# Optimization experiments

Hardware: AMD Instinct MI355X
Metric: run time of the kernel (lower is better)

The kernel has to match this reference:

```python
import jax, jax.numpy as jnp
import numpy as np

D_IN = 1024
D_OUT = 1024
NUM_HEADS = 16
HEAD_DIM = D_OUT // NUM_HEADS


def setup_inputs() -> dict:
    key = jax.random.key(0)
    ks = jax.random.split(key, 6)
    s = 0.02
    return {
        "x": jax.random.normal(ks[0], (4, 2048, D_IN), dtype=jnp.float32),
        "Wq": jax.random.normal(ks[1], (D_IN, D_OUT), dtype=jnp.float32) * s,
        "Wk": jax.random.normal(ks[2], (D_IN, D_OUT), dtype=jnp.float32) * s,
        "Wv": jax.random.normal(ks[3], (D_IN, D_OUT), dtype=jnp.float32) * s,
        "Wo": jax.random.normal(ks[4], (D_OUT, D_OUT), dtype=jnp.float32) * s,
        "bo": jax.random.normal(ks[5], (D_OUT,), dtype=jnp.float32) * s,
    }


def reference(x, Wq, Wk, Wv, Wo, bo):
    B, T, _ = x.shape
    H, Dh = NUM_HEADS, HEAD_DIM
    # projections -> [B, H, T, Dh]
    q = (x @ Wq).reshape(B, T, H, Dh).transpose(0, 2, 1, 3)
    k = (x @ Wk).reshape(B, T, H, Dh).transpose(0, 2, 1, 3)
    v = (x @ Wv).reshape(B, T, H, Dh).transpose(0, 2, 1, 3)
    # scores [B, H, T, T]
    scores = jnp.einsum('bhqd,bhkd->bhqk', q, k)
    causal = jnp.triu(jnp.ones((T, T), dtype=bool), k=1)
    scores = jnp.where(causal, -jnp.inf, scores)
    attn = jax.nn.softmax(scores / jnp.sqrt(jnp.float32(Dh)), axis=-1)
    # dropout=0.0 -> identity
    ctx = jnp.einsum('bhqk,bhkd->bhqd', attn, v)
    ctx = ctx.transpose(0, 2, 1, 3).reshape(B, T, H * Dh)
    return ctx @ Wo + bo
```

## Files before the change

### kernel.cpp

```cpp
#include <hip/hip_runtime.h>
#include <hip/hip_bf16.h>
#include <stdint.h>

#define TSEQ 2048
#define DMODEL 1024

typedef __attribute__((ext_vector_type(8))) short bf16x8;
typedef __attribute__((ext_vector_type(4))) float f32x4;
typedef __attribute__((ext_vector_type(16))) float f32x16;

union Frag { bf16x8 v; uint4 q; };

__device__ __forceinline__ uint16_t f2bfu(float f) {
  uint32_t u = __builtin_bit_cast(uint32_t, f);
  u += 0x7fffu + ((u >> 16) & 1u);
  return (uint16_t)(u >> 16);
}

__device__ __forceinline__ uint32_t pk2bf(float a, float b) {
  return ((uint32_t)f2bfu(b) << 16) | f2bfu(a);
}

__device__ __forceinline__ float fexp2(float x) {
#if __has_builtin(__builtin_amdgcn_exp2f)
  return __builtin_amdgcn_exp2f(x);
#else
  return exp2f(x);
#endif
}

__device__ __forceinline__ void gload_lds16(const void* g, void* l) {
  __builtin_amdgcn_global_load_lds(
      (const __attribute__((address_space(1))) void*)g,
      (__attribute__((address_space(3))) void*)l, 16, 0, 0);
}


__global__ __launch_bounds__(256) void cvt_x_kernel(const float* __restrict__ x,
                                                    uint16_t* __restrict__ xb, int n4) {
  int i = blockIdx.x * 256 + threadIdx.x;
  if (i >= n4) return;
  float4 v = ((const float4*)x)[i];
  ushort4 o;
  o.x = f2bfu(v.x); o.y = f2bfu(v.y); o.z = f2bfu(v.z); o.w = f2bfu(v.w);
  ((ushort4*)xb)[i] = o;
}

__global__ __launch_bounds__(256) void cvt_w_kernel(const float* __restrict__ Wq,
    const float* __restrict__ Wk, const float* __restrict__ Wv, const float* __restrict__ Wo,
    uint16_t* __restrict__ Wqkvt, uint16_t* __restrict__ Wot) {
  const float* src = (blockIdx.z == 0) ? Wq : (blockIdx.z == 1) ? Wk
                   : (blockIdx.z == 2) ? Wv : Wo;
  uint16_t* dst = (blockIdx.z < 3) ? (Wqkvt + (size_t)blockIdx.z * DMODEL * DMODEL) : Wot;
  const float wscale = (blockIdx.z == 0) ? 0.125f * 1.4426950408889634f : 1.0f;
  __shared__ float tile[32][33];
  const int x0 = blockIdx.x * 32, y0 = blockIdx.y * 32;
  for (int ii = 0; ii < 4; ii++) {
    int i = threadIdx.y + ii * 8;
    tile[i][threadIdx.x] = src[(size_t)(y0 + i) * DMODEL + x0 + threadIdx.x];
  }
  __syncthreads();
  for (int ii = 0; ii < 4; ii++) {
    int i = threadIdx.y + ii * 8;
    dst[(size_t)(x0 + i) * DMODEL + y0 + threadIdx.x] = f2bfu(tile[threadIdx.x][i] * wscale);
  }
}


__device__ __forceinline__ void g8_stage_p1(const char* Ab, int kb, char* ldsA, int tid) {
#pragma unroll
  for (int r = 0; r < 3; ++r) {
    const int u = tid + r * 512;
    const int row = u >> 3;
    const int sc = ((u & 7) * 16) ^ ((row & 7) << 4);
    gload_lds16(Ab + (size_t)row * 2048 + kb + sc, ldsA + u * 16);
  }
}

__device__ __forceinline__ void g8_stage_p2(const char* Ab, const char* Bb, int kb,
                                            char* ldsA, char* ldsB, int tid) {
  {
    const int u = tid + 3 * 512;
    const int row = u >> 3;
    const int sc = ((u & 7) * 16) ^ ((row & 7) << 4);
    gload_lds16(Ab + (size_t)row * 2048 + kb + sc, ldsA + u * 16);
  }
#pragma unroll
  for (int r = 0; r < 2; ++r) {
    const int u = tid + r * 512;
    const int row = u >> 3;
    const int sc = ((u & 7) * 16) ^ ((row & 7) << 4);
    gload_lds16(Bb + (size_t)row * 2048 + kb + sc, ldsB + u * 16);
  }
}

__device__ __forceinline__ void gemm256x128_core(const char* Ab, const char* Bb,
                                                 char* lds,
                                                 f32x4 (&acc)[4][4]) {
  const int tid = threadIdx.x;
  const int lane = tid & 63;
  const int w = tid >> 6;
  const int lr = lane & 15, lg = lane >> 4;
  const int wmb = (w >> 1) * 64;
  const int wnb = (w & 1) * 64;
  char* const A0 = lds;
  char* const A1 = lds + 32768;
  char* const B0 = lds + 65536;
  char* const B1 = lds + 81920;

#pragma unroll
  for (int i = 0; i < 4; i++)
#pragma unroll
    for (int j = 0; j < 4; j++) acc[i][j] = (f32x4){0.f, 0.f, 0.f, 0.f};

  g8_stage_p1(Ab, 0, A0, tid);
  g8_stage_p2(Ab, Bb, 0, A0, B0, tid);
  for (int t = 0; t < 16; ++t) {
    const char* At = (t & 1) ? A1 : A0;
    const char* Bt = (t & 1) ? B1 : B0;
    char* nA = (t & 1) ? A0 : A1;
    char* nB = (t & 1) ? B0 : B1;
    if (t + 1 < 16) {
      g8_stage_p1(Ab, (t + 1) * 128, nA, tid);
      asm volatile("s_waitcnt vmcnt(3)" ::: "memory");
    } else {
      asm volatile("s_waitcnt vmcnt(0)" ::: "memory");
    }
    __builtin_amdgcn_s_barrier();
    __builtin_amdgcn_sched_barrier(0);

    Frag bf0[4], bf1[4];
#pragma unroll
    for (int ni = 0; ni < 4; ni++) {
      const int row = wnb + ni * 16 + lr;
      const int swz = (row & 7) << 4;
      bf0[ni].q = *(const uint4*)(Bt + row * 128 + ((lg * 16) ^ swz));
      bf1[ni].q = *(const uint4*)(Bt + row * 128 + ((64 + lg * 16) ^ swz));
    }
    Frag pa0[2], pa1[2];
#pragma unroll
    for (int mi = 0; mi < 2; mi++) {
      const int row = wmb + mi * 16 + lr;
      const int swz = (row & 7) << 4;
      pa0[mi].q = *(const uint4*)(At + row * 128 + ((lg * 16) ^ swz));
      pa1[mi].q = *(const uint4*)(At + row * 128 + ((64 + lg * 16) ^ swz));
    }
    __builtin_amdgcn_s_setprio(1);
#pragma unroll
    for (int mi = 0; mi < 2; mi++)
#pragma unroll
      for (int ni = 0; ni < 4; ni++) {
        acc[mi][ni] = __builtin_amdgcn_mfma_f32_16x16x32_bf16(pa0[mi].v, bf0[ni].v,
                                                              acc[mi][ni], 0, 0, 0);
        acc[mi][ni] = __builtin_amdgcn_mfma_f32_16x16x32_bf16(pa1[mi].v, bf1[ni].v,
                                                              acc[mi][ni], 0, 0, 0);
      }
    __builtin_amdgcn_s_setprio(0);

    if (t + 1 < 16) g8_stage_p2(Ab, Bb, (t + 1) * 128, nA, nB, tid);
#pragma unroll
    for (int mi = 2; mi < 4; mi++) {
      const int row = wmb + mi * 16 + lr;
      const int swz = (row & 7) << 4;
      Frag qa0, qa1;
      qa0.q = *(const uint4*)(At + row * 128 + ((lg * 16) ^ swz));
      qa1.q = *(const uint4*)(At + row * 128 + ((64 + lg * 16) ^ swz));
      __builtin_amdgcn_s_setprio(1);
#pragma unroll
      for (int ni = 0; ni < 4; ni++) {
        acc[mi][ni] = __builtin_amdgcn_mfma_f32_16x16x32_bf16(qa0.v, bf0[ni].v,
                                                              acc[mi][ni], 0, 0, 0);
        acc[mi][ni] = __builtin_amdgcn_mfma_f32_16x16x32_bf16(qa1.v, bf1[ni].v,
                                                              acc[mi][ni], 0, 0, 0);
      }
      __builtin_amdgcn_s_setprio(0);
    }
    __builtin_amdgcn_s_barrier();
  }
}


__global__ __launch_bounds__(512, 2) void gemm_qkv_kernel(const uint16_t* __restrict__ Xb,
    const uint16_t* __restrict__ Wt, uint16_t* __restrict__ Qo,
    uint16_t* __restrict__ Ko, uint16_t* __restrict__ Vt) {
  __shared__ __align__(16) char lds[98304];
  const int m0 = (blockIdx.x & 31) * 256;
  const int n0 = (blockIdx.x >> 5) * 128;
  f32x4 acc[4][4];
  gemm256x128_core((const char*)Xb + (size_t)m0 * 2048, (const char*)Wt + (size_t)n0 * 2048,
                   lds, acc);

  const int tid = threadIdx.x, w = tid >> 6, lane = tid & 63;
  const int lr = lane & 15, lg = lane >> 4;
  const int wmb = (w >> 1) * 64, wnb = (w & 1) * 64;

  if (n0 >= 2048) {
    char* vr = lds + (w & 1) * 33792;
#pragma unroll
    for (int mi = 0; mi < 4; mi++)
#pragma unroll
      for (int ni = 0; ni < 4; ni++) {
        const int d = ni * 16 + lr;
        const int tl = wmb + mi * 16 + 4 * lg;
        uint2 pr;
        pr.x = pk2bf(acc[mi][ni][0], acc[mi][ni][1]);
        pr.y = pk2bf(acc[mi][ni][2], acc[mi][ni][3]);
        *(uint2*)(vr + d * 528 + tl * 2) = pr;
      }
    __syncthreads();
    const int bb = m0 >> 11, t0 = m0 & 2047;
    const int h0 = (n0 - 2048) >> 6;
#pragma unroll
    for (int j = 0; j < 8; j++) {
      const int linear = (tid + j * 512) * 16;
      const int rg = linear >> 15;
      const int rem = linear & 32767;
      const int d = rem >> 9;
      const int toff = rem & 511;
      const uint4 val = *(const uint4*)(lds + rg * 33792 + d * 528 + toff);
      const int bh = bb * 16 + h0 + rg;
      *(uint4*)((char*)Vt + ((size_t)(bh * 64 + d) * TSEQ + t0) * 2 + toff) = val;
    }
  } else {
#pragma unroll
    for (int mi = 0; mi < 4; mi++)
#pragma unroll
      for (int ni = 0; ni < 4; ni++) {
        const int col = n0 + wnb + ni * 16 + lr;
        const int p = col >> 10, c = col & 1023, h = c >> 6, d = c & 63;
#pragma unroll
        for (int r = 0; r < 4; r++) {
          const int row = m0 + wmb + mi * 16 + 4 * lg + r;
          const int bb = row >> 11, t = row & 2047;
          const int bh = bb * 16 + h;
          const uint16_t val = f2bfu(acc[mi][ni][r]);
          if (p == 0) Qo[((size_t)bh * TSEQ + t) * 64 + d] = val;
          else        Ko[((size_t)bh * TSEQ + t) * 64 + d] = val;
        }
      }
  }
}


__device__ __forceinline__ void stage_kv(const char* Kb, const char* Vb, int kv0,
                                         char* kdst, char* vdst, int tid) {
  const int w1024 = (tid >> 6) * 1024;
#pragma unroll
  for (int i = 0; i < 2; i++) {
    const int o = i * 4096 + tid * 16;
    const int row = o >> 7;
    const int scol = (o & 127) ^ ((row & 7) << 4);
    gload_lds16(Kb + (size_t)(kv0 + row) * 128 + scol, kdst + i * 4096 + w1024);
    gload_lds16(Vb + (size_t)row * 4096 + kv0 * 2 + scol, vdst + i * 4096 + w1024);
  }
}

__global__ __launch_bounds__(256, 3) void attn_kernel(const uint16_t* __restrict__ Qw,
    const uint16_t* __restrict__ Kw, const uint16_t* __restrict__ Vtw,
    uint16_t* __restrict__ Ctx) {
  const int bid = blockIdx.x;
  const int qt = 15 - (bid >> 6);
  const int bh = bid & 63;
  const int tid = threadIdx.x;
  const int w = tid >> 6, lane = tid & 63;
  const int lq = lane & 31;
  const int hi = lane >> 5;
  const int wq0 = qt * 128 + w * 32;

  const char* Qb = (const char*)Qw + (size_t)bh * TSEQ * 128;
  const char* Kb = (const char*)Kw + (size_t)bh * TSEQ * 128;
  const char* Vb = (const char*)Vtw + (size_t)bh * 64 * 4096;

  __shared__ __align__(16) char kbuf[2][8192];
  __shared__ __align__(16) char vbuf[2][8192];

  Frag qa[4];
#pragma unroll
  for (int kc = 0; kc < 4; kc++)
    qa[kc].q = *(const uint4*)(Qb + (size_t)(wq0 + lq) * 128 + kc * 32 + hi * 16);

  f32x16 o0 = 0.f, o1 = 0.f;
  float mrun = -1e30f, lrun = 0.f;

  const int nt = 2 * qt + 2;
  stage_kv(Kb, Vb, 0, kbuf[0], vbuf[0], tid);
  int cur = 0;
  for (int t = 0; t < nt; ++t) {
    const int kv0 = t * 64;
    if (t + 1 < nt) {
      stage_kv(Kb, Vb, kv0 + 64, kbuf[cur ^ 1], vbuf[cur ^ 1], tid);
      asm volatile("s_waitcnt vmcnt(4)" ::: "memory");
    } else {
      asm volatile("s_waitcnt vmcnt(0)" ::: "memory");
    }
    __builtin_amdgcn_s_barrier();
    __builtin_amdgcn_sched_barrier(0);

    if (kv0 <= wq0 + 31) {
      const char* Kt = kbuf[cur];
      const char* Vt = vbuf[cur];
      f32x16 s[2];
#pragma unroll
      for (int kvh = 0; kvh < 2; kvh++) {
        f32x16 acc = 0.f;
#pragma unroll
        for (int kc = 0; kc < 4; kc++) {
          const int row = kvh * 32 + lq;
          Frag kf;
          kf.q = *(const uint4*)(Kt + row * 128 + ((kc * 32 + hi * 16) ^ ((row & 7) << 4)));
          acc = __builtin_amdgcn_mfma_f32_32x32x16_bf16(kf.v, qa[kc].v, acc, 0, 0, 0);
        }
        s[kvh] = acc;
      }
      if (kv0 + 63 > wq0) {
        const int q_abs = wq0 + lq;
#pragma unroll
        for (int kvh = 0; kvh < 2; kvh++)
#pragma unroll
          for (int r = 0; r < 16; r++) {
            const int kv_abs = kv0 + kvh * 32 + (r & 3) + 8 * (r >> 2) + 4 * hi;
            if (kv_abs > q_abs) s[kvh][r] = -1e30f;
          }
      }
      float mt = s[0][0];
#pragma unroll
      for (int r = 1; r < 16; r++) mt = fmaxf(mt, s[0][r]);
#pragma unroll
      for (int r = 0; r < 16; r++) mt = fmaxf(mt, s[1][r]);
      mt = fmaxf(mt, __shfl_xor(mt, 32));
      const float mnew = fmaxf(mrun, mt);
      const float corr = fexp2(mrun - mnew);
      mrun = mnew;
#pragma unroll
      for (int kvh = 0; kvh < 2; kvh++)
#pragma unroll
        for (int r = 0; r < 16; r++) s[kvh][r] = fexp2(s[kvh][r] - mnew);
      float ps = 0.f;
#pragma unroll
      for (int kvh = 0; kvh < 2; kvh++)
#pragma unroll
        for (int r = 0; r < 16; r++) ps += s[kvh][r];
      ps += __shfl_xor(ps, 32);
      lrun = lrun * corr + ps;
      o0 *= corr;
      o1 *= corr;
      uint32_t pk[2][8];
#pragma unroll
      for (int kvh = 0; kvh < 2; kvh++)
#pragma unroll
        for (int j = 0; j < 8; j++)
          pk[kvh][j] = pk2bf(s[kvh][2 * j], s[kvh][2 * j + 1]);
#pragma unroll
      for (int c16 = 0; c16 < 4; c16++) {
        const int kvh = c16 >> 1, cl = c16 & 1;
        const uint32_t s0 = (uint32_t)__shfl_xor((int)pk[kvh][4 * cl + 0], 32);
        const uint32_t s1 = (uint32_t)__shfl_xor((int)pk[kvh][4 * cl + 1], 32);
        const uint32_t s2 = (uint32_t)__shfl_xor((int)pk[kvh][4 * cl + 2], 32);
        const uint32_t s3 = (uint32_t)__shfl_xor((int)pk[kvh][4 * cl + 3], 32);
        Frag pb;
        pb.q.x = hi ? s2 : pk[kvh][4 * cl + 0];
        pb.q.y = hi ? s3 : pk[kvh][4 * cl + 1];
        pb.q.z = hi ? pk[kvh][4 * cl + 2] : s0;
        pb.q.w = hi ? pk[kvh][4 * cl + 3] : s1;
#pragma unroll
        for (int dblk = 0; dblk < 2; dblk++) {
          const int row = dblk * 32 + lq;
          Frag vf;
          vf.q = *(const uint4*)(Vt + row * 128 + ((c16 * 32 + hi * 16) ^ ((row & 7) << 4)));
          if (dblk == 0)
            o0 = __builtin_amdgcn_mfma_f32_32x32x16_bf16(vf.v, pb.v, o0, 0, 0, 0);
          else
            o1 = __builtin_amdgcn_mfma_f32_32x32x16_bf16(vf.v, pb.v, o1, 0, 0, 0);
        }
      }
    }
    __builtin_amdgcn_s_barrier();
    cur ^= 1;
  }

  const int bb = bh >> 4, hh = bh & 15;
  const float inv = 1.0f / lrun;
  const int q_abs = wq0 + lq;
  uint16_t* crow = Ctx + ((size_t)bb * TSEQ + q_abs) * DMODEL + hh * 64;
#pragma unroll
  for (int dblk = 0; dblk < 2; dblk++)
#pragma unroll
    for (int g = 0; g < 4; g++) {
      const float a0 = (dblk ? o1[4 * g + 0] : o0[4 * g + 0]) * inv;
      const float a1 = (dblk ? o1[4 * g + 1] : o0[4 * g + 1]) * inv;
      const float a2 = (dblk ? o1[4 * g + 2] : o0[4 * g + 2]) * inv;
      const float a3 = (dblk ? o1[4 * g + 3] : o0[4 * g + 3]) * inv;
      uint2 st;
      st.x = pk2bf(a0, a1);
      st.y = pk2bf(a2, a3);
      *(uint2*)(crow + dblk * 32 + 8 * g + 4 * hi) = st;
    }
}


__global__ __launch_bounds__(512, 2) void gemm_out_kernel(const uint16_t* __restrict__ Cb,
    const uint16_t* __restrict__ Wot, const float* __restrict__ bo,
    float* __restrict__ out) {
  __shared__ __align__(16) char lds[98304];
  const int m0 = (blockIdx.x & 31) * 256;
  const int n0 = (blockIdx.x >> 5) * 128;
  f32x4 acc[4][4];
  gemm256x128_core((const char*)Cb + (size_t)m0 * 2048, (const char*)Wot + (size_t)n0 * 2048,
                   lds, acc);

  const int tid = threadIdx.x, w = tid >> 6, lane = tid & 63;
  const int lr = lane & 15, lg = lane >> 4;
  const int wmb = (w >> 1) * 64, wnb = (w & 1) * 64;
#pragma unroll
  for (int mi = 0; mi < 4; mi++)
#pragma unroll
    for (int ni = 0; ni < 4; ni++) {
      const int col = n0 + wnb + ni * 16 + lr;
      const float bias = bo[col];
#pragma unroll
      for (int r = 0; r < 4; r++) {
        const int row = m0 + wmb + mi * 16 + 4 * lg + r;
        out[(size_t)row * DMODEL + col] = acc[mi][ni][r] + bias;
      }
    }
}


extern "C" void kernel_launch(void* const* d_in, const int* in_sizes, int n_in,
                              void* d_out, int out_size, void* d_ws, size_t ws_size,
                              hipStream_t stream) {
  const float* x  = (const float*)d_in[0];
  const float* Wq = (const float*)d_in[1];
  const float* Wk = (const float*)d_in[2];
  const float* Wv = (const float*)d_in[3];
  const float* Wo = (const float*)d_in[4];
  const float* bo = (const float*)d_in[5];
  float* out = (float*)d_out;

  char* ws = (char*)d_ws;
  uint16_t* Xb    = (uint16_t*)(ws);
  uint16_t* Ctx   = (uint16_t*)(ws);
  uint16_t* Wqkvt = (uint16_t*)(ws + (16u << 20));
  uint16_t* Wot   = (uint16_t*)(ws + (22u << 20));
  uint16_t* Qw    = (uint16_t*)(ws + (24u << 20));
  uint16_t* Kw    = (uint16_t*)(ws + (40u << 20));
  uint16_t* Vtw   = (uint16_t*)(ws + (56u << 20));
  (void)ws_size; (void)in_sizes; (void)n_in; (void)out_size;

  cvt_x_kernel<<<8192, 256, 0, stream>>>(x, Xb, 2097152);
  cvt_w_kernel<<<dim3(32, 32, 4), dim3(32, 8), 0, stream>>>(Wq, Wk, Wv, Wo, Wqkvt, Wot);
  gemm_qkv_kernel<<<768, 512, 0, stream>>>(Xb, Wqkvt, Qw, Kw, Vtw);
  attn_kernel<<<1024, 256, 0, stream>>>(Qw, Kw, Vtw, Ctx);
  gemm_out_kernel<<<256, 512, 0, stream>>>(Ctx, Wot, bo, out);
}
```

Baseline: 185.4 us.

## Split QKV projection into 256x256-tile Q/K GEMM and separate V GEMM

Replaces the single fused QKV GEMM launch, which used 256x128 tiles, with two launches. The Q/K part uses a new 256x256 tile core with 8 waves, 128KB of double-buffered LDS and 32 accumulators per wave, which raises arithmetic intensity and reuse of each staged tile. The V part keeps the old 256x128 core and its transposed store path. This drops the per-block branch on output type and gives each GEMM a tile shape suited to its epilogue. In exchange it adds an extra kernel launch, and the larger tile brings more register and LDS pressure, which may limit occupancy. The Q/K grid is 256 blocks, which may underfill the GPU.

```diff
diff --git a/kernel.cpp b/kernel.cpp
--- a/kernel.cpp
+++ b/kernel.cpp
@@ -64,6 +64,121 @@
     int i = threadIdx.y + ii * 8;
     dst[(size_t)(x0 + i) * DMODEL + y0 + threadIdx.x] = f2bfu(tile[threadIdx.x][i] * wscale);
   }
+}
+
+__device__ __forceinline__ void stage256(const char* Gb, int kb, char* ldsT, int tid) {
+#pragma unroll
+  for (int r = 0; r < 4; ++r) {
+    const int u = tid + r * 512;
+    const int row = u >> 3;
+    const int sc = ((u & 7) * 16) ^ ((row & 7) << 4);
+    gload_lds16(Gb + (size_t)row * 2048 + kb + sc, ldsT + u * 16);
+  }
+}
+
+
+__device__ __forceinline__ void gemm256sq_core(const char* Ab, const char* Bb,
+                                               char* lds,
+                                               f32x4 (&acc)[8][4]) {
+  const int tid = threadIdx.x;
+  const int lane = tid & 63;
+  const int w = tid >> 6;
+  const int lr = lane & 15, lg = lane >> 4;
+  const int wmb = (w >> 2) * 128;
+  const int wnb = (w & 3) * 64;
+  char* const A0 = lds;
+  char* const A1 = lds + 32768;
+  char* const B0 = lds + 65536;
+  char* const B1 = lds + 98304;
+
+#pragma unroll
+  for (int i = 0; i < 8; i++)
+#pragma unroll
+    for (int j = 0; j < 4; j++) acc[i][j] = (f32x4){0.f, 0.f, 0.f, 0.f};
+
+  stage256(Ab, 0, A0, tid);
+  stage256(Bb, 0, B0, tid);
+  for (int t = 0; t < 16; ++t) {
+    const char* At = (t & 1) ? A1 : A0;
+    const char* Bt = (t & 1) ? B1 : B0;
+    char* nA = (t & 1) ? A0 : A1;
+    char* nB = (t & 1) ? B0 : B1;
+    if (t + 1 < 16) {
+      stage256(Ab, (t + 1) * 128, nA, tid);
+      asm volatile("s_waitcnt vmcnt(4)" ::: "memory");
+    } else {
+      asm volatile("s_waitcnt vmcnt(0)" ::: "memory");
+    }
+    __builtin_amdgcn_s_barrier();
+    __builtin_amdgcn_sched_barrier(0);
+
+    Frag bf0[4], bf1[4];
+#pragma unroll
+    for (int ni = 0; ni < 4; ni++) {
+      const int row = wnb + ni * 16 + lr;
+      const int swz = (row & 7) << 4;
+      bf0[ni].q = *(const uint4*)(Bt + row * 128 + ((lg * 16) ^ swz));
+      bf1[ni].q = *(const uint4*)(Bt + row * 128 + ((64 + lg * 16) ^ swz));
+    }
+#pragma unroll
+    for (int ph = 0; ph < 4; ph++) {
+      Frag a0[2], a1[2];
+#pragma unroll
+      for (int i = 0; i < 2; i++) {
+        const int row = wmb + (2 * ph + i) * 16 + lr;
+        const int swz = (row & 7) << 4;
+        a0[i].q = *(const uint4*)(At + row * 128 + ((lg * 16) ^ swz));
+        a1[i].q = *(const uint4*)(At + row * 128 + ((64 + lg * 16) ^ swz));
+      }
+      __builtin_amdgcn_s_setprio(1);
+#pragma unroll
+      for (int i = 0; i < 2; i++) {
+        const int mi = 2 * ph + i;
+#pragma unroll
+        for (int ni = 0; ni < 4; ni++) {
+          acc[mi][ni] = __builtin_amdgcn_mfma_f32_16x16x32_bf16(a0[i].v, bf0[ni].v,
+                                                                acc[mi][ni], 0, 0, 0);
+          acc[mi][ni] = __builtin_amdgcn_mfma_f32_16x16x32_bf16(a1[i].v, bf1[ni].v,
+                                                                acc[mi][ni], 0, 0, 0);
+        }
+      }
+      __builtin_amdgcn_s_setprio(0);
+      if (ph == 0 && t + 1 < 16) stage256(Bb, (t + 1) * 128, nB, tid);
+    }
+    __builtin_amdgcn_s_barrier();
+  }
+}
+
+
+__global__ __launch_bounds__(512, 2) void gemm_qk_kernel(const uint16_t* __restrict__ Xb,
+    const uint16_t* __restrict__ Wt, uint16_t* __restrict__ Qo,
+    uint16_t* __restrict__ Ko) {
+  __shared__ __align__(16) char lds[131072];
+  const int m0 = (blockIdx.x & 31) * 256;
+  const int n0 = (blockIdx.x >> 5) * 256;
+  f32x4 acc[8][4];
+  gemm256sq_core((const char*)Xb + (size_t)m0 * 2048, (const char*)Wt + (size_t)n0 * 2048,
+                 lds, acc);
+
+  const int tid = threadIdx.x, w = tid >> 6, lane = tid & 63;
+  const int lr = lane & 15, lg = lane >> 4;
+  const int wmb = (w >> 2) * 128, wnb = (w & 3) * 64;
+#pragma unroll
+  for (int mi = 0; mi < 8; mi++)
+#pragma unroll
+    for (int ni = 0; ni < 4; ni++) {
+      const int col = n0 + wnb + ni * 16 + lr;
+      const int p = col >> 10, c = col & 1023, h = c >> 6, d = c & 63;
+#pragma unroll
+      for (int r = 0; r < 4; r++) {
+        const int row = m0 + wmb + mi * 16 + 4 * lg + r;
+        const int bb = row >> 11, t = row & 2047;
+        const int bh = bb * 16 + h;
+        const uint16_t val = f2bfu(acc[mi][ni][r]);
+        if (p == 0) Qo[((size_t)bh * TSEQ + t) * 64 + d] = val;
+        else        Ko[((size_t)bh * TSEQ + t) * 64 + d] = val;
+      }
+    }
 }
 
 
@@ -180,64 +295,44 @@
 }
 
 
-__global__ __launch_bounds__(512, 2) void gemm_qkv_kernel(const uint16_t* __restrict__ Xb,
-    const uint16_t* __restrict__ Wt, uint16_t* __restrict__ Qo,
-    uint16_t* __restrict__ Ko, uint16_t* __restrict__ Vt) {
+__global__ __launch_bounds__(512, 2) void gemm_v_kernel(const uint16_t* __restrict__ Xb,
+    const uint16_t* __restrict__ Wtv, uint16_t* __restrict__ Vt) {
   __shared__ __align__(16) char lds[98304];
   const int m0 = (blockIdx.x & 31) * 256;
   const int n0 = (blockIdx.x >> 5) * 128;
   f32x4 acc[4][4];
-  gemm256x128_core((const char*)Xb + (size_t)m0 * 2048, (const char*)Wt + (size_t)n0 * 2048,
+  gemm256x128_core((const char*)Xb + (size_t)m0 * 2048, (const char*)Wtv + (size_t)n0 * 2048,
                    lds, acc);
 
   const int tid = threadIdx.x, w = tid >> 6, lane = tid & 63;
   const int lr = lane & 15, lg = lane >> 4;
-  const int wmb = (w >> 1) * 64, wnb = (w & 1) * 64;
-
-  if (n0 >= 2048) {
-    char* vr = lds + (w & 1) * 33792;
-#pragma unroll
-    for (int mi = 0; mi < 4; mi++)
-#pragma unroll
-      for (int ni = 0; ni < 4; ni++) {
-        const int d = ni * 16 + lr;
-        const int tl = wmb + mi * 16 + 4 * lg;
-        uint2 pr;
-        pr.x = pk2bf(acc[mi][ni][0], acc[mi][ni][1]);
-        pr.y = pk2bf(acc[mi][ni][2], acc[mi][ni][3]);
-        *(uint2*)(vr + d * 528 + tl * 2) = pr;
-      }
-    __syncthreads();
-    const int bb = m0 >> 11, t0 = m0 & 2047;
-    const int h0 = (n0 - 2048) >> 6;
-#pragma unroll
-    for (int j = 0; j < 8; j++) {
-      const int linear = (tid + j * 512) * 16;
-      const int rg = linear >> 15;
-      const int rem = linear & 32767;
-      const int d = rem >> 9;
-      const int toff = rem & 511;
-      const uint4 val = *(const uint4*)(lds + rg * 33792 + d * 528 + toff);
-      const int bh = bb * 16 + h0 + rg;
-      *(uint4*)((char*)Vt + ((size_t)(bh * 64 + d) * TSEQ + t0) * 2 + toff) = val;
-    }
-  } else {
-#pragma unroll
-    for (int mi = 0; mi < 4; mi++)
-#pragma unroll
-      for (int ni = 0; ni < 4; ni++) {
-        const int col = n0 + wnb + ni * 16 + lr;
-        const int p = col >> 10, c = col & 1023, h = c >> 6, d = c & 63;
-#pragma unroll
-        for (int r = 0; r < 4; r++) {
-          const int row = m0 + wmb + mi * 16 + 4 * lg + r;
-          const int bb = row >> 11, t = row & 2047;
-          const int bh = bb * 16 + h;
-          const uint16_t val = f2bfu(acc[mi][ni][r]);
-          if (p == 0) Qo[((size_t)bh * TSEQ + t) * 64 + d] = val;
-          else        Ko[((size_t)bh * TSEQ + t) * 64 + d] = val;
-        }
-      }
+  const int wmb = (w >> 1) * 64;
+
+  char* vr = lds + (w & 1) * 33792;
+#pragma unroll
+  for (int mi = 0; mi < 4; mi++)
+#pragma unroll
+    for (int ni = 0; ni < 4; ni++) {
+      const int d = ni * 16 + lr;
+      const int tl = wmb + mi * 16 + 4 * lg;
+      uint2 pr;
+      pr.x = pk2bf(acc[mi][ni][0], acc[mi][ni][1]);
+      pr.y = pk2bf(acc[mi][ni][2], acc[mi][ni][3]);
+      *(uint2*)(vr + d * 528 + tl * 2) = pr;
+    }
+  __syncthreads();
+  const int bb = m0 >> 11, t0 = m0 & 2047;
+  const int h0 = n0 >> 6;
+#pragma unroll
+  for (int j = 0; j < 8; j++) {
+    const int linear = (tid + j * 512) * 16;
+    const int rg = linear >> 15;
+    const int rem = linear & 32767;
+    const int d = rem >> 9;
+    const int toff = rem & 511;
+    const uint4 val = *(const uint4*)(lds + rg * 33792 + d * 528 + toff);
+    const int bh = bb * 16 + h0 + rg;
+    *(uint4*)((char*)Vt + ((size_t)(bh * 64 + d) * TSEQ + t0) * 2 + toff) = val;
   }
 }
 
@@ -449,7 +544,8 @@
 
   cvt_x_kernel<<<8192, 256, 0, stream>>>(x, Xb, 2097152);
   cvt_w_kernel<<<dim3(32, 32, 4), dim3(32, 8), 0, stream>>>(Wq, Wk, Wv, Wo, Wqkvt, Wot);
-  gemm_qkv_kernel<<<768, 512, 0, stream>>>(Xb, Wqkvt, Qw, Kw, Vtw);
+  gemm_qk_kernel<<<256, 512, 0, stream>>>(Xb, Wqkvt, Qw, Kw);
+  gemm_v_kernel<<<256, 512, 0, stream>>>(Xb, Wqkvt + (size_t)2048 * 1024, Vtw);
   attn_kernel<<<1024, 256, 0, stream>>>(Qw, Kw, Vtw, Ctx);
   gemm_out_kernel<<<256, 512, 0, stream>>>(Ctx, Wot, bo, out);
 }
```

Result: faster. 176.2 us (-5.0%).
